# Kernel tuning notes

Hardware: AMD Instinct MI355X
Metric: run time of the kernel (lower is better)

## Reference

```python
import jax, jax.numpy as jnp
import numpy as np

NHEAD = 8
K_NEIGH = 16


def setup_inputs() -> dict:
    key = jax.random.key(0)
    ks = jax.random.split(key, 6)
    B, L, D = 4, 4096, 512
    x = jax.random.normal(ks[0], (B, L, D), dtype=jnp.float32)
    positions = jax.random.uniform(ks[1], (B, L, 3), dtype=jnp.float32)
    in_proj_w = jax.random.normal(ks[2], (3 * D, D), dtype=jnp.float32) * 0.02
    in_proj_b = jax.random.normal(ks[3], (3 * D,), dtype=jnp.float32) * 0.02
    out_proj_w = jax.random.normal(ks[4], (D, D), dtype=jnp.float32) * 0.02
    out_proj_b = jax.random.normal(ks[5], (D,), dtype=jnp.float32) * 0.02
    return {"x": x, "positions": positions, "in_proj_w": in_proj_w,
            "in_proj_b": in_proj_b, "out_proj_w": out_proj_w, "out_proj_b": out_proj_b}


def _sparse_attention(x, positions, in_proj_w, in_proj_b, out_proj_w, out_proj_b):
    B, L, D = x.shape
    H, dh = NHEAD, D // NHEAD
    K = min(K_NEIGH, L)
    scale = 1.0 / jnp.sqrt(jnp.asarray(dh, x.dtype))

    # Pairwise distances [B, L, L]; topk smallest -> neighbor indices [B, L, K].
    diff = positions[:, :, None, :] - positions[:, None, :, :]
    dist = jnp.sqrt(jnp.sum(diff * diff, axis=-1))
    _, nbr = jax.lax.top_k(-dist, K)  # [B, L, K]

    Wq, Wk, Wv = in_proj_w[:D], in_proj_w[D:2 * D], in_proj_w[2 * D:]
    bq, bk, bv = in_proj_b[:D], in_proj_b[D:2 * D], in_proj_b[2 * D:]

    # Query is x[b, i] itself (self is always its own nearest neighbor at dist 0),
    # so the selected attention row equals attention with query x[b, i] over neighbors.
    q = ((x @ Wq.T + bq) * scale).reshape(B, L, H, dh)

    # Gather neighbor features: [B, L, K, D]
    b_idx = jnp.arange(B)[:, None, None]
    local_x = x[b_idx, nbr]
    k = (local_x @ Wk.T + bk).reshape(B, L, K, H, dh)
    v = (local_x @ Wv.T + bv).reshape(B, L, K, H, dh)

    scores = jnp.einsum('blhd,blkhd->blhk', q, k)
    attn = jax.nn.softmax(scores, axis=-1)
    ctx = jnp.einsum('blhk,blkhd->blhd', attn, v).reshape(B, L, D)
    out = ctx @ out_proj_w.T + out_proj_b

    # Faithful fallback: if i not among its neighbors, pass through x[b, i].
    is_in = jnp.any(nbr == jnp.arange(L)[None, :, None], axis=-1)  # [B, L]
    return jnp.where(is_in[..., None], out, x)


def reference(x, positions, in_proj_w, in_proj_b, out_proj_w, out_proj_b):
    return _sparse_attention(x, positions, in_proj_w, in_proj_b, out_proj_w, out_proj_b)
```

## Files before the change

### kernel.cpp

```cpp
#include <hip/hip_runtime.h>
#include <cfloat>
#include <cmath>

constexpr int B = 4;
constexpr int L = 4096;
constexpr int D = 512;
constexpr int NH = 8;
constexpr int DH = 64;
constexpr int KN = 16;
constexpr int M = B * L;
constexpr int N_IN = 3 * D;
constexpr int NCELL = 512;

typedef __attribute__((ext_vector_type(8))) short short8;
typedef __attribute__((ext_vector_type(4))) float f32x4;
typedef unsigned short ushort;
typedef unsigned long long ull;

__device__ __forceinline__ ushort f2bf(float f) {
  unsigned u = __float_as_uint(f);
  u = u + 0x7fffu + ((u >> 16) & 1u);
  return (ushort)(u >> 16);
}
__device__ __forceinline__ float bf2f(ushort h) {
  return __uint_as_float(((unsigned)h) << 16);
}
__device__ __forceinline__ float dot8(const uint4 qu, const uint4 ku, float a) {
  a = fmaf(bf2f((ushort)qu.x), bf2f((ushort)ku.x), a);
  a = fmaf(bf2f((ushort)(qu.x >> 16)), bf2f((ushort)(ku.x >> 16)), a);
  a = fmaf(bf2f((ushort)qu.y), bf2f((ushort)ku.y), a);
  a = fmaf(bf2f((ushort)(qu.y >> 16)), bf2f((ushort)(ku.y >> 16)), a);
  a = fmaf(bf2f((ushort)qu.z), bf2f((ushort)ku.z), a);
  a = fmaf(bf2f((ushort)(qu.z >> 16)), bf2f((ushort)(ku.z >> 16)), a);
  a = fmaf(bf2f((ushort)qu.w), bf2f((ushort)ku.w), a);
  a = fmaf(bf2f((ushort)(qu.w >> 16)), bf2f((ushort)(ku.w >> 16)), a);
  return a;
}
__device__ __forceinline__ void acc8(float wgt, const uint4 vv, float (&acc)[8]) {
  acc[0] = fmaf(wgt, bf2f((ushort)vv.x), acc[0]);
  acc[1] = fmaf(wgt, bf2f((ushort)(vv.x >> 16)), acc[1]);
  acc[2] = fmaf(wgt, bf2f((ushort)vv.y), acc[2]);
  acc[3] = fmaf(wgt, bf2f((ushort)(vv.y >> 16)), acc[3]);
  acc[4] = fmaf(wgt, bf2f((ushort)vv.z), acc[4]);
  acc[5] = fmaf(wgt, bf2f((ushort)(vv.z >> 16)), acc[5]);
  acc[6] = fmaf(wgt, bf2f((ushort)vv.w), acc[6]);
  acc[7] = fmaf(wgt, bf2f((ushort)(vv.w >> 16)), acc[7]);
}
__device__ __forceinline__ uint2 pack4hi(const float4 v) {
  uint2 o;
  o.x = (unsigned)f2bf(v.x) | ((unsigned)f2bf(v.y) << 16);
  o.y = (unsigned)f2bf(v.z) | ((unsigned)f2bf(v.w) << 16);
  return o;
}
__device__ __forceinline__ void gload16(const void* g, void* l) {
  __builtin_amdgcn_global_load_lds(
      (const __attribute__((address_space(1))) void*)g,
      (__attribute__((address_space(3))) void*)l, 16, 0, 0);
}
__device__ __forceinline__ int morton3(int x, int y, int z) {
  int m = 0;
#pragma unroll
  for (int i = 0; i < 3; ++i)
    m |= (((x >> i) & 1) << (3 * i + 2)) | (((y >> i) & 1) << (3 * i + 1)) |
         (((z >> i) & 1) << (3 * i));
  return m;
}

constexpr int TP = 65;

__device__ __forceinline__ void topk_finish(
    const float* sxT, const float* syT, const float* szT, ull* lstw,
    const int lane, const float qx, const float qy, const float qz,
    const unsigned mbits, const int l, const int row,
    int* __restrict__ nbr, int* __restrict__ isin) {
  unsigned lo = 1, hi = 0x40400001u;
  while (lo < hi) {
    const unsigned mid = (lo + hi) >> 1;
    const int c = __popcll(__ballot(mbits < mid));
    if (c >= 16) hi = mid; else lo = mid + 1;
  }
  const unsigned P = lo + 16;

  int cnt = 0;
  ull am = __ballot(mbits < P);
  const ull below = (1ull << lane) - 1ull;
  while (am) {
    const int pl = (int)__builtin_ctzll(am);
    am &= am - 1;
    const int a = pl * TP + lane;
    const float dx = qx - sxT[a], dy = qy - syT[a], dz = qz - szT[a];
    const float d2 = fmaf(dx, dx, fmaf(dy, dy, dz * dz));
    const bool hit = __float_as_uint(d2) < P;
    const ull msk = __ballot(hit);
    if (hit) {
      const int slot = cnt + __popcll(msk & below);
      if (slot < 64) {
        const unsigned c = (unsigned)(lane * 64 + pl);
        lstw[slot] = ((ull)__float_as_uint(sqrtf(d2)) << 32) | c;
      }
    }
    cnt += __popcll(msk);
  }
  const int n = min(cnt, 64);

  const ull mine = (lane < n) ? lstw[lane] : ~0ull;
  int r = 0;
  for (int i = 0; i < n; ++i) r += (lstw[i] < mine) ? 1 : 0;

  const int idx = (int)(unsigned)(mine & 0xffffffffu);
  const bool wr = (lane < n) && (r < 16);
  if (wr) nbr[(size_t)row * KN + r] = idx;
  const ull hit2 = __ballot(wr && idx == l);
  if (lane == 0) isin[row] = hit2 ? 1 : 0;
}

constexpr int TOPK_BLKS = B * (L / 32);
constexpr int SORT_BLKS = B;
constexpr int CVTX_BLKS = 1024;
constexpr int CVTW_BLKS = 256;
constexpr int STAGE0_BLKS = TOPK_BLKS + SORT_BLKS + CVTX_BLKS + CVTW_BLKS;

__global__ __launch_bounds__(512) void stage0_kernel(
    const float* __restrict__ pos, const float* __restrict__ x,
    const float* __restrict__ in_w, const float* __restrict__ out_w,
    int* __restrict__ nbr, int* __restrict__ isin, int* __restrict__ qorder,
    ushort* __restrict__ xb, ushort* __restrict__ iwh,
    ushort* __restrict__ owh, ushort* __restrict__ owl) {
  __shared__ ull smem_u64[54016 / 8];

  const int bid = blockIdx.x;
  const int tid = threadIdx.x;

  if (bid < TOPK_BLKS) {
    float* sxT = (float*)smem_u64;
    float* syT = sxT + 64 * TP;
    float* szT = syT + 64 * TP;
    ull* lst = (ull*)(szT + 64 * TP);

    const int wave = tid >> 6;
    const int lane = tid & 63;
    const int b = bid >> 7;
    const int l0 = (bid & 127) * 32 + wave * 4;

    const float* p = pos + (size_t)b * L * 3;
    for (int i = tid; i < L; i += 512) {
      const int a = (i & 63) * TP + (i >> 6);
      sxT[a] = p[3 * i + 0];
      syT[a] = p[3 * i + 1];
      szT[a] = p[3 * i + 2];
    }
    __syncthreads();

    float qx[4], qy[4], qz[4], mn[4];
#pragma unroll
    for (int q = 0; q < 4; ++q) {
      const int lq = l0 + q;
      const int qa = (lq & 63) * TP + (lq >> 6);
      qx[q] = sxT[qa];
      qy[q] = syT[qa];
      qz[q] = szT[qa];
      mn[q] = FLT_MAX;
    }

    const int base = lane * TP;
    for (int j = 0; j < 64; ++j) {
      const int a = base + j;
      const float cx = sxT[a], cy = syT[a], cz = szT[a];
#pragma unroll
      for (int q = 0; q < 4; ++q) {
        const float dx = qx[q] - cx, dy = qy[q] - cy, dz = qz[q] - cz;
        mn[q] = fminf(mn[q], fmaf(dx, dx, fmaf(dy, dy, dz * dz)));
      }
    }

    ull* lstw = lst + wave * 64;
#pragma unroll
    for (int q = 0; q < 4; ++q)
      topk_finish(sxT, syT, szT, lstw, lane, qx[q], qy[q], qz[q],
                  __float_as_uint(mn[q]), l0 + q, b * L + l0 + q, nbr, isin);

  } else if (bid < TOPK_BLKS + SORT_BLKS) {
    int* hist = (int*)smem_u64;
    int* scanbuf = hist + NCELL;
    const int b = bid - TOPK_BLKS;
    const int t = tid;
    hist[t] = 0;
    __syncthreads();

    int cells[8], ranks[8];
    const float* p = pos + (size_t)b * L * 3;
#pragma unroll
    for (int q = 0; q < 8; ++q) {
      const int i = q * 512 + t;
      const int ix = min(7, max(0, (int)(p[3 * i + 0] * 8.f)));
      const int iy = min(7, max(0, (int)(p[3 * i + 1] * 8.f)));
      const int iz = min(7, max(0, (int)(p[3 * i + 2] * 8.f)));
      cells[q] = morton3(ix, iy, iz);
      ranks[q] = atomicAdd(&hist[cells[q]], 1);
    }
    __syncthreads();

    int accv = hist[t];
    const int orig = accv;
    scanbuf[t] = accv;
    __syncthreads();
    for (int s = 1; s < NCELL; s <<= 1) {
      const int o = (t >= s) ? scanbuf[t - s] : 0;
      __syncthreads();
      accv += o;
      scanbuf[t] = accv;
      __syncthreads();
    }
    hist[t] = accv - orig;
    __syncthreads();

#pragma unroll
    for (int q = 0; q < 8; ++q) {
      const int i = q * 512 + t;
      qorder[b * L + hist[cells[q]] + ranks[q]] = i;
    }

  } else if (bid < TOPK_BLKS + SORT_BLKS + CVTX_BLKS) {
    const int vb = bid - TOPK_BLKS - SORT_BLKS;
    const int n8 = M * D / 8;
    for (int i = vb * 512 + tid; i < n8; i += CVTX_BLKS * 512) {
      const float4 v0 = reinterpret_cast<const float4*>(x)[i * 2];
      const float4 v1 = reinterpret_cast<const float4*>(x)[i * 2 + 1];
      uint4 o;
      const uint2 a = pack4hi(v0), b2 = pack4hi(v1);
      o.x = a.x; o.y = a.y; o.z = b2.x; o.w = b2.y;
      reinterpret_cast<uint4*>(xb)[i] = o;
    }

  } else {
    const int vb = bid - TOPK_BLKS - SORT_BLKS - CVTX_BLKS;
    const int ni8 = N_IN * D / 8;
    const int no8 = D * D / 8;
    for (int i = vb * 512 + tid; i < ni8 + no8; i += CVTW_BLKS * 512) {
      if (i < ni8) {
        const float4 v0 = reinterpret_cast<const float4*>(in_w)[i * 2];
        const float4 v1 = reinterpret_cast<const float4*>(in_w)[i * 2 + 1];
        uint4 o;
        const uint2 a = pack4hi(v0), b2 = pack4hi(v1);
        o.x = a.x; o.y = a.y; o.z = b2.x; o.w = b2.y;
        reinterpret_cast<uint4*>(iwh)[i] = o;
      } else {
        const int j = i - ni8;
        const float4 v0 = reinterpret_cast<const float4*>(out_w)[j * 2];
        const float4 v1 = reinterpret_cast<const float4*>(out_w)[j * 2 + 1];
        uint4 oh, ol;
        const uint2 a = pack4hi(v0), b2 = pack4hi(v1);
        oh.x = a.x; oh.y = a.y; oh.z = b2.x; oh.w = b2.y;
        const float4 r0 = make_float4(v0.x - bf2f(f2bf(v0.x)), v0.y - bf2f(f2bf(v0.y)),
                                      v0.z - bf2f(f2bf(v0.z)), v0.w - bf2f(f2bf(v0.w)));
        const float4 r1 = make_float4(v1.x - bf2f(f2bf(v1.x)), v1.y - bf2f(f2bf(v1.y)),
                                      v1.z - bf2f(f2bf(v1.z)), v1.w - bf2f(f2bf(v1.w)));
        const uint2 c = pack4hi(r0), d2 = pack4hi(r1);
        ol.x = c.x; ol.y = c.y; ol.z = d2.x; ol.w = d2.y;
        reinterpret_cast<uint4*>(owh)[j] = oh;
        reinterpret_cast<uint4*>(owl)[j] = ol;
      }
    }
  }
}

constexpr int BM = 128, BN = 128;
constexpr int BK2 = 64;

__global__ __launch_bounds__(256) void gemm_in(const ushort* __restrict__ A,
                                               const ushort* __restrict__ W,
                                               const float* __restrict__ bias,
                                               ushort* __restrict__ qb,
                                               ushort* __restrict__ kb,
                                               ushort* __restrict__ vb) {
  __shared__ ushort Ah[BM * BK2];
  __shared__ ushort Bh[BN * BK2];

  const int tid = threadIdx.x;
  const int m0 = blockIdx.x * BM;
  const int n0 = blockIdx.y * BN;

  const int wv = tid >> 6;
  const int lane = tid & 63;
  const int srow0 = wv * 8 + (lane >> 3);
  const int gchunk = (lane & 7) ^ (lane >> 3);
  const ushort* Asrc = A + (size_t)(m0 + srow0) * D + gchunk * 8;
  const ushort* Wsrc = W + (size_t)(n0 + srow0) * D + gchunk * 8;
  ushort* AhB0 = Ah + (wv * 8) * BK2;
  ushort* AhB1 = Ah + (wv * 8 + 32) * BK2;
  ushort* AhB2 = Ah + (wv * 8 + 64) * BK2;
  ushort* AhB3 = Ah + (wv * 8 + 96) * BK2;
  ushort* BhB0 = Bh + (wv * 8) * BK2;
  ushort* BhB1 = Bh + (wv * 8 + 32) * BK2;
  ushort* BhB2 = Bh + (wv * 8 + 64) * BK2;
  ushort* BhB3 = Bh + (wv * 8 + 96) * BK2;

  const int wr0 = (wv >> 1) * 64;
  const int wc0 = (wv & 1) * 64;
  const int fr_row = lane & 15;
  const int cbase = lane >> 4;
  const int rx = lane & 7;

  f32x4 acc[4][4];
#pragma unroll
  for (int i = 0; i < 4; ++i)
#pragma unroll
    for (int j = 0; j < 4; ++j) acc[i][j] = {0.f, 0.f, 0.f, 0.f};

  for (int k0 = 0; k0 < D; k0 += BK2) {
    __syncthreads();
    gload16(Asrc + k0, AhB0);
    gload16(Asrc + (size_t)32 * D + k0, AhB1);
    gload16(Asrc + (size_t)64 * D + k0, AhB2);
    gload16(Asrc + (size_t)96 * D + k0, AhB3);
    gload16(Wsrc + k0, BhB0);
    gload16(Wsrc + (size_t)32 * D + k0, BhB1);
    gload16(Wsrc + (size_t)64 * D + k0, BhB2);
    gload16(Wsrc + (size_t)96 * D + k0, BhB3);
    __syncthreads();

#pragma unroll
    for (int kk = 0; kk < 2; ++kk) {
      const int slot = (kk * 4 + cbase) ^ rx;
      short8 ah[4];
#pragma unroll
      for (int fr = 0; fr < 4; ++fr)
        ah[fr] = *reinterpret_cast<const short8*>(
            &Ah[(wr0 + fr * 16 + fr_row) * BK2 + slot * 8]);
#pragma unroll
      for (int fc = 0; fc < 4; ++fc) {
        const short8 bh = *reinterpret_cast<const short8*>(
            &Bh[(wc0 + fc * 16 + fr_row) * BK2 + slot * 8]);
#pragma unroll
        for (int fr = 0; fr < 4; ++fr)
          acc[fr][fc] = __builtin_amdgcn_mfma_f32_16x16x32_bf16(ah[fr], bh, acc[fr][fc], 0, 0, 0);
      }
    }
  }

  const int region = n0 >> 9;
  ushort* outb = region == 0 ? qb : (region == 1 ? kb : vb);
  const float scl = region == 0 ? 0.125f : 1.0f;
  const int nloc0 = (n0 & 511) + wc0;
#pragma unroll
  for (int fr = 0; fr < 4; ++fr) {
#pragma unroll
    for (int r = 0; r < 4; ++r) {
      const int grow = m0 + wr0 + fr * 16 + (lane >> 4) * 4 + r;
#pragma unroll
      for (int fc = 0; fc < 4; ++fc) {
        const int cc = fc * 16 + (lane & 15);
        const float v = (acc[fr][fc][r] + bias[n0 + wc0 + cc]) * scl;
        outb[(size_t)grow * D + nloc0 + cc] = f2bf(v);
      }
    }
  }
}

__global__ __launch_bounds__(256) void gemm_out(const ushort* __restrict__ A,
                                                const ushort* __restrict__ Wh,
                                                const ushort* __restrict__ Wl,
                                                const float* __restrict__ bias,
                                                float* __restrict__ C,
                                                const float* __restrict__ X,
                                                const int* __restrict__ isin) {
  __shared__ ushort Ah[BM * BK2];
  __shared__ ushort Bh[BN * BK2];
  __shared__ ushort Bl[BN * BK2];

  const int tid = threadIdx.x;
  const int m0 = blockIdx.x * BM;
  const int n0 = blockIdx.y * BN;

  const int wv = tid >> 6;
  const int lane = tid & 63;
  const int srow0 = wv * 8 + (lane >> 3);
  const int gchunk = (lane & 7) ^ (lane >> 3);
  const ushort* Asrc = A + (size_t)(m0 + srow0) * D + gchunk * 8;
  const ushort* Hsrc = Wh + (size_t)(n0 + srow0) * D + gchunk * 8;
  const ushort* Lsrc = Wl + (size_t)(n0 + srow0) * D + gchunk * 8;
  ushort* AhB0 = Ah + (wv * 8) * BK2;
  ushort* AhB1 = Ah + (wv * 8 + 32) * BK2;
  ushort* AhB2 = Ah + (wv * 8 + 64) * BK2;
  ushort* AhB3 = Ah + (wv * 8 + 96) * BK2;
  ushort* BhB0 = Bh + (wv * 8) * BK2;
  ushort* BhB1 = Bh + (wv * 8 + 32) * BK2;
  ushort* BhB2 = Bh + (wv * 8 + 64) * BK2;
  ushort* BhB3 = Bh + (wv * 8 + 96) * BK2;
  ushort* BlB0 = Bl + (wv * 8) * BK2;
  ushort* BlB1 = Bl + (wv * 8 + 32) * BK2;
  ushort* BlB2 = Bl + (wv * 8 + 64) * BK2;
  ushort* BlB3 = Bl + (wv * 8 + 96) * BK2;

  const int wr0 = (wv >> 1) * 64;
  const int wc0 = (wv & 1) * 64;
  const int fr_row = lane & 15;
  const int cbase = lane >> 4;
  const int rx = lane & 7;

  f32x4 acc[4][4];
#pragma unroll
  for (int i = 0; i < 4; ++i)
#pragma unroll
    for (int j = 0; j < 4; ++j) acc[i][j] = {0.f, 0.f, 0.f, 0.f};

  for (int k0 = 0; k0 < D; k0 += BK2) {
    __syncthreads();
    gload16(Asrc + k0, AhB0);
    gload16(Asrc + (size_t)32 * D + k0, AhB1);
    gload16(Asrc + (size_t)64 * D + k0, AhB2);
    gload16(Asrc + (size_t)96 * D + k0, AhB3);
    gload16(Hsrc + k0, BhB0);
    gload16(Hsrc + (size_t)32 * D + k0, BhB1);
    gload16(Hsrc + (size_t)64 * D + k0, BhB2);
    gload16(Hsrc + (size_t)96 * D + k0, BhB3);
    gload16(Lsrc + k0, BlB0);
    gload16(Lsrc + (size_t)32 * D + k0, BlB1);
    gload16(Lsrc + (size_t)64 * D + k0, BlB2);
    gload16(Lsrc + (size_t)96 * D + k0, BlB3);
    __syncthreads();

#pragma unroll
    for (int kk = 0; kk < 2; ++kk) {
      const int slot = (kk * 4 + cbase) ^ rx;
      short8 ah[4];
#pragma unroll
      for (int fr = 0; fr < 4; ++fr)
        ah[fr] = *reinterpret_cast<const short8*>(
            &Ah[(wr0 + fr * 16 + fr_row) * BK2 + slot * 8]);
#pragma unroll
      for (int fc = 0; fc < 4; ++fc) {
        const short8 bh = *reinterpret_cast<const short8*>(
            &Bh[(wc0 + fc * 16 + fr_row) * BK2 + slot * 8]);
        const short8 bl = *reinterpret_cast<const short8*>(
            &Bl[(wc0 + fc * 16 + fr_row) * BK2 + slot * 8]);
#pragma unroll
        for (int fr = 0; fr < 4; ++fr) {
          acc[fr][fc] = __builtin_amdgcn_mfma_f32_16x16x32_bf16(ah[fr], bh, acc[fr][fc], 0, 0, 0);
          acc[fr][fc] = __builtin_amdgcn_mfma_f32_16x16x32_bf16(ah[fr], bl, acc[fr][fc], 0, 0, 0);
        }
      }
    }
  }

#pragma unroll
  for (int fr = 0; fr < 4; ++fr) {
#pragma unroll
    for (int r = 0; r < 4; ++r) {
      const int grow = m0 + wr0 + fr * 16 + (lane >> 4) * 4 + r;
      const int ok = isin[grow];
#pragma unroll
      for (int fc = 0; fc < 4; ++fc) {
        const int gcol = n0 + wc0 + fc * 16 + (lane & 15);
        float v = acc[fr][fc][r] + bias[gcol];
        if (!ok) v = X[(size_t)grow * D + gcol];
        C[(size_t)grow * D + gcol] = v;
      }
    }
  }
}

__global__ __launch_bounds__(256) void attn_kernel(const ushort* __restrict__ qb,
                                                   const ushort* __restrict__ kb,
                                                   const ushort* __restrict__ vb,
                                                   const int* __restrict__ nbr,
                                                   const int* __restrict__ qorder,
                                                   ushort* __restrict__ ctx) {
  const int wave = threadIdx.x >> 6;
  const int lane = threadIdx.x & 63;
  const int xcd = blockIdx.x & 7;
  const int chunk = blockIdx.x >> 3;
  const int b = xcd >> 1;
  const int slot = ((xcd & 1) * 512 + chunk) * 4 + wave;
  const int l = qorder[b * L + slot];
  const int bl = b * L + l;
  const int bbase = b * L;
  const int* nb = nbr + (size_t)bl * KN;

  const int h = lane >> 3;
  const int n0 = lane & 7;
  const int glane = h * 8;

  const ushort* qp = qb + (size_t)bl * D + h * DH;
  uint4 qv[8];
#pragma unroll
  for (int i = 0; i < 8; ++i)
    qv[i] = *reinterpret_cast<const uint4*>(qp + i * 8);

  const int j0 = nb[n0];
  const int j1 = nb[n0 + 8];
  float a0 = 0.f, a1 = 0.f;
  {
    const ushort* kr0 = kb + (size_t)(bbase + j0) * D + h * DH;
    const ushort* kr1 = kb + (size_t)(bbase + j1) * D + h * DH;
#pragma unroll
    for (int i = 0; i < 8; ++i) {
      a0 = dot8(qv[i], *reinterpret_cast<const uint4*>(kr0 + i * 8), a0);
      a1 = dot8(qv[i], *reinterpret_cast<const uint4*>(kr1 + i * 8), a1);
    }
  }

  float mx = fmaxf(a0, a1);
  mx = fmaxf(mx, __shfl_xor(mx, 1));
  mx = fmaxf(mx, __shfl_xor(mx, 2));
  mx = fmaxf(mx, __shfl_xor(mx, 4));
  const float e0 = expf(a0 - mx), e1 = expf(a1 - mx);
  float sm = e0 + e1;
  sm += __shfl_xor(sm, 1);
  sm += __shfl_xor(sm, 2);
  sm += __shfl_xor(sm, 4);
  const float inv = 1.0f / sm;
  const float w0 = e0 * inv, w1 = e1 * inv;

  float ww[KN];
  int jj[KN];
#pragma unroll
  for (int n = 0; n < KN; ++n) {
    const int src = glane + (n & 7);
    ww[n] = __shfl((n < 8) ? w0 : w1, src);
    jj[n] = __shfl((n < 8) ? j0 : j1, src);
  }

  const int d0 = n0 * 8;
  const ushort* vbase = vb + (size_t)bbase * D + h * DH + d0;
  float acc[8];
#pragma unroll
  for (int i = 0; i < 8; ++i) acc[i] = 0.f;

#pragma unroll
  for (int g = 0; g < KN; g += 4) {
    const uint4 va0 = *reinterpret_cast<const uint4*>(vbase + (size_t)jj[g] * D);
    const uint4 va1 = *reinterpret_cast<const uint4*>(vbase + (size_t)jj[g + 1] * D);
    const uint4 va2 = *reinterpret_cast<const uint4*>(vbase + (size_t)jj[g + 2] * D);
    const uint4 va3 = *reinterpret_cast<const uint4*>(vbase + (size_t)jj[g + 3] * D);
    acc8(ww[g], va0, acc);
    acc8(ww[g + 1], va1, acc);
    acc8(ww[g + 2], va2, acc);
    acc8(ww[g + 3], va3, acc);
  }

  uint4 o;
  o.x = (unsigned)f2bf(acc[0]) | ((unsigned)f2bf(acc[1]) << 16);
  o.y = (unsigned)f2bf(acc[2]) | ((unsigned)f2bf(acc[3]) << 16);
  o.z = (unsigned)f2bf(acc[4]) | ((unsigned)f2bf(acc[5]) << 16);
  o.w = (unsigned)f2bf(acc[6]) | ((unsigned)f2bf(acc[7]) << 16);
  *reinterpret_cast<uint4*>(ctx + (size_t)bl * D + h * DH + d0) = o;
}

extern "C" void kernel_launch(void* const* d_in, const int* in_sizes, int n_in,
                              void* d_out, int out_size, void* d_ws, size_t ws_size,
                              hipStream_t stream) {
  const float* x     = (const float*)d_in[0];
  const float* pos   = (const float*)d_in[1];
  const float* in_w  = (const float*)d_in[2];
  const float* in_b  = (const float*)d_in[3];
  const float* out_w = (const float*)d_in[4];
  const float* out_b = (const float*)d_in[5];
  float* out = (float*)d_out;

  const size_t nbr_bytes  = (size_t)M * KN * sizeof(int);
  const size_t isin_bytes = (size_t)M * sizeof(int);
  const size_t half_bytes = (size_t)M * D * sizeof(ushort);
  const size_t iwh_bytes  = (size_t)N_IN * D * sizeof(ushort);
  const size_t ow_bytes   = (size_t)D * D * sizeof(ushort);
  const size_t sort_bytes = (size_t)M * sizeof(int);
  const size_t need = nbr_bytes + isin_bytes + 5 * half_bytes +
                      iwh_bytes + 2 * ow_bytes + sort_bytes + 16384;
  if (ws_size < need) return;

  char* w = (char*)d_ws;
  int*    nbr    = (int*)w;    w += (nbr_bytes + 255) & ~(size_t)255;
  int*    isin   = (int*)w;    w += (isin_bytes + 255) & ~(size_t)255;
  ushort* xb     = (ushort*)w; w += (half_bytes + 255) & ~(size_t)255;
  ushort* qb     = (ushort*)w; w += (half_bytes + 255) & ~(size_t)255;
  ushort* kb     = (ushort*)w; w += (half_bytes + 255) & ~(size_t)255;
  ushort* vb     = (ushort*)w; w += (half_bytes + 255) & ~(size_t)255;
  ushort* ctxb   = (ushort*)w; w += (half_bytes + 255) & ~(size_t)255;
  ushort* iwh    = (ushort*)w; w += (iwh_bytes + 255) & ~(size_t)255;
  ushort* owh    = (ushort*)w; w += (ow_bytes + 255) & ~(size_t)255;
  ushort* owl    = (ushort*)w; w += (ow_bytes + 255) & ~(size_t)255;
  int*    qorder = (int*)w;

  stage0_kernel<<<STAGE0_BLKS, 512, 0, stream>>>(
      pos, x, in_w, out_w, nbr, isin, qorder, xb, iwh, owh, owl);

  gemm_in<<<dim3(M / BM, N_IN / BN), 256, 0, stream>>>(xb, iwh, in_b, qb, kb, vb);

  attn_kernel<<<M / 4, 256, 0, stream>>>(qb, kb, vb, nbr, qorder, ctxb);

  gemm_out<<<dim3(M / BM, D / BN), 256, 0, stream>>>(ctxb, owh, owl, out_b, out, x, isin);
}
```

Before: 145.5 us.

## Move top-k neighbor search into the QKV projection GEMM kernel launch

The kNN top-k blocks move out of the stage0 conversion kernel and into a merged kernel alongside the input-projection GEMM blocks. Top-k now runs with 256-thread blocks covering 16 rows each, so it overlaps with the GEMM instead of with the conversion work. The goal is to balance the stages and hide the compute-bound top-k behind the GEMM. The catch is that the merged kernel has the top-k's larger shared-memory footprint and the union of both paths' register needs, which can lower GEMM occupancy.

```diff
diff --git a/kernel.cpp b/kernel.cpp
--- a/kernel.cpp
+++ b/kernel.cpp
@@ -114,75 +114,25 @@
   if (lane == 0) isin[row] = hit2 ? 1 : 0;
 }
 
-constexpr int TOPK_BLKS = B * (L / 32);
 constexpr int SORT_BLKS = B;
 constexpr int CVTX_BLKS = 1024;
 constexpr int CVTW_BLKS = 256;
-constexpr int STAGE0_BLKS = TOPK_BLKS + SORT_BLKS + CVTX_BLKS + CVTW_BLKS;
+constexpr int STAGE0_BLKS = SORT_BLKS + CVTX_BLKS + CVTW_BLKS;
 
 __global__ __launch_bounds__(512) void stage0_kernel(
     const float* __restrict__ pos, const float* __restrict__ x,
     const float* __restrict__ in_w, const float* __restrict__ out_w,
-    int* __restrict__ nbr, int* __restrict__ isin, int* __restrict__ qorder,
-    ushort* __restrict__ xb, ushort* __restrict__ iwh,
-    ushort* __restrict__ owh, ushort* __restrict__ owl) {
-  __shared__ ull smem_u64[54016 / 8];
+    int* __restrict__ qorder, ushort* __restrict__ xb,
+    ushort* __restrict__ iwh, ushort* __restrict__ owh,
+    ushort* __restrict__ owl) {
+  __shared__ int hist[NCELL];
+  __shared__ int scanbuf[NCELL];
 
   const int bid = blockIdx.x;
   const int tid = threadIdx.x;
 
-  if (bid < TOPK_BLKS) {
-    float* sxT = (float*)smem_u64;
-    float* syT = sxT + 64 * TP;
-    float* szT = syT + 64 * TP;
-    ull* lst = (ull*)(szT + 64 * TP);
-
-    const int wave = tid >> 6;
-    const int lane = tid & 63;
-    const int b = bid >> 7;
-    const int l0 = (bid & 127) * 32 + wave * 4;
-
-    const float* p = pos + (size_t)b * L * 3;
-    for (int i = tid; i < L; i += 512) {
-      const int a = (i & 63) * TP + (i >> 6);
-      sxT[a] = p[3 * i + 0];
-      syT[a] = p[3 * i + 1];
-      szT[a] = p[3 * i + 2];
-    }
-    __syncthreads();
-
-    float qx[4], qy[4], qz[4], mn[4];
-#pragma unroll
-    for (int q = 0; q < 4; ++q) {
-      const int lq = l0 + q;
-      const int qa = (lq & 63) * TP + (lq >> 6);
-      qx[q] = sxT[qa];
-      qy[q] = syT[qa];
-      qz[q] = szT[qa];
-      mn[q] = FLT_MAX;
-    }
-
-    const int base = lane * TP;
-    for (int j = 0; j < 64; ++j) {
-      const int a = base + j;
-      const float cx = sxT[a], cy = syT[a], cz = szT[a];
-#pragma unroll
-      for (int q = 0; q < 4; ++q) {
-        const float dx = qx[q] - cx, dy = qy[q] - cy, dz = qz[q] - cz;
-        mn[q] = fminf(mn[q], fmaf(dx, dx, fmaf(dy, dy, dz * dz)));
-      }
-    }
-
-    ull* lstw = lst + wave * 64;
-#pragma unroll
-    for (int q = 0; q < 4; ++q)
-      topk_finish(sxT, syT, szT, lstw, lane, qx[q], qy[q], qz[q],
-                  __float_as_uint(mn[q]), l0 + q, b * L + l0 + q, nbr, isin);
-
-  } else if (bid < TOPK_BLKS + SORT_BLKS) {
-    int* hist = (int*)smem_u64;
-    int* scanbuf = hist + NCELL;
-    const int b = bid - TOPK_BLKS;
+  if (bid < SORT_BLKS) {
+    const int b = bid;
     const int t = tid;
     hist[t] = 0;
     __syncthreads();
@@ -220,8 +170,8 @@
       qorder[b * L + hist[cells[q]] + ranks[q]] = i;
     }
 
-  } else if (bid < TOPK_BLKS + SORT_BLKS + CVTX_BLKS) {
-    const int vb = bid - TOPK_BLKS - SORT_BLKS;
+  } else if (bid < SORT_BLKS + CVTX_BLKS) {
+    const int vb = bid - SORT_BLKS;
     const int n8 = M * D / 8;
     for (int i = vb * 512 + tid; i < n8; i += CVTX_BLKS * 512) {
       const float4 v0 = reinterpret_cast<const float4*>(x)[i * 2];
@@ -233,7 +183,7 @@
     }
 
   } else {
-    const int vb = bid - TOPK_BLKS - SORT_BLKS - CVTX_BLKS;
+    const int vb = bid - SORT_BLKS - CVTX_BLKS;
     const int ni8 = N_IN * D / 8;
     const int no8 = D * D / 8;
     for (int i = vb * 512 + tid; i < ni8 + no8; i += CVTW_BLKS * 512) {
@@ -266,92 +216,150 @@
 
 constexpr int BM = 128, BN = 128;
 constexpr int BK2 = 64;
-
-__global__ __launch_bounds__(256) void gemm_in(const ushort* __restrict__ A,
-                                               const ushort* __restrict__ W,
-                                               const float* __restrict__ bias,
-                                               ushort* __restrict__ qb,
-                                               ushort* __restrict__ kb,
-                                               ushort* __restrict__ vb) {
-  __shared__ ushort Ah[BM * BK2];
-  __shared__ ushort Bh[BN * BK2];
-
+constexpr int TOPK_BLKS = B * (L / 16);
+constexpr int GEMM_BLKS = (M / BM) * (N_IN / BN);
+constexpr int K1_BLKS = TOPK_BLKS + GEMM_BLKS;
+
+__global__ __launch_bounds__(256) void topk_gemm_kernel(
+    const float* __restrict__ pos, const ushort* __restrict__ A,
+    const ushort* __restrict__ W, const float* __restrict__ bias,
+    int* __restrict__ nbr, int* __restrict__ isin,
+    ushort* __restrict__ qb, ushort* __restrict__ kb,
+    ushort* __restrict__ vb) {
+  __shared__ ull smem_u64[51968 / 8];
+
+  const int bid = blockIdx.x;
   const int tid = threadIdx.x;
-  const int m0 = blockIdx.x * BM;
-  const int n0 = blockIdx.y * BN;
-
-  const int wv = tid >> 6;
-  const int lane = tid & 63;
-  const int srow0 = wv * 8 + (lane >> 3);
-  const int gchunk = (lane & 7) ^ (lane >> 3);
-  const ushort* Asrc = A + (size_t)(m0 + srow0) * D + gchunk * 8;
-  const ushort* Wsrc = W + (size_t)(n0 + srow0) * D + gchunk * 8;
-  ushort* AhB0 = Ah + (wv * 8) * BK2;
-  ushort* AhB1 = Ah + (wv * 8 + 32) * BK2;
-  ushort* AhB2 = Ah + (wv * 8 + 64) * BK2;
-  ushort* AhB3 = Ah + (wv * 8 + 96) * BK2;
-  ushort* BhB0 = Bh + (wv * 8) * BK2;
-  ushort* BhB1 = Bh + (wv * 8 + 32) * BK2;
-  ushort* BhB2 = Bh + (wv * 8 + 64) * BK2;
-  ushort* BhB3 = Bh + (wv * 8 + 96) * BK2;
-
-  const int wr0 = (wv >> 1) * 64;
-  const int wc0 = (wv & 1) * 64;
-  const int fr_row = lane & 15;
-  const int cbase = lane >> 4;
-  const int rx = lane & 7;
-
-  f32x4 acc[4][4];
-#pragma unroll
-  for (int i = 0; i < 4; ++i)
-#pragma unroll
-    for (int j = 0; j < 4; ++j) acc[i][j] = {0.f, 0.f, 0.f, 0.f};
-
-  for (int k0 = 0; k0 < D; k0 += BK2) {
+
+  if (bid < TOPK_BLKS) {
+    float* sxT = (float*)smem_u64;
+    float* syT = sxT + 64 * TP;
+    float* szT = syT + 64 * TP;
+    ull* lst = (ull*)(szT + 64 * TP);
+
+    const int wave = tid >> 6;
+    const int lane = tid & 63;
+    const int b = bid >> 8;
+    const int l0 = (bid & 255) * 16 + wave * 4;
+
+    const float* p = pos + (size_t)b * L * 3;
+    for (int i = tid; i < L; i += 256) {
+      const int a = (i & 63) * TP + (i >> 6);
+      sxT[a] = p[3 * i + 0];
+      syT[a] = p[3 * i + 1];
+      szT[a] = p[3 * i + 2];
+    }
     __syncthreads();
-    gload16(Asrc + k0, AhB0);
-    gload16(Asrc + (size_t)32 * D + k0, AhB1);
-    gload16(Asrc + (size_t)64 * D + k0, AhB2);
-    gload16(Asrc + (size_t)96 * D + k0, AhB3);
-    gload16(Wsrc + k0, BhB0);
-    gload16(Wsrc + (size_t)32 * D + k0, BhB1);
-    gload16(Wsrc + (size_t)64 * D + k0, BhB2);
-    gload16(Wsrc + (size_t)96 * D + k0, BhB3);
-    __syncthreads();
-
-#pragma unroll
-    for (int kk = 0; kk < 2; ++kk) {
-      const int slot = (kk * 4 + cbase) ^ rx;
-      short8 ah[4];
-#pragma unroll
-      for (int fr = 0; fr < 4; ++fr)
-        ah[fr] = *reinterpret_cast<const short8*>(
-            &Ah[(wr0 + fr * 16 + fr_row) * BK2 + slot * 8]);
-#pragma unroll
-      for (int fc = 0; fc < 4; ++fc) {
-        const short8 bh = *reinterpret_cast<const short8*>(
-            &Bh[(wc0 + fc * 16 + fr_row) * BK2 + slot * 8]);
+
+    float qx[4], qy[4], qz[4], mn[4];
+#pragma unroll
+    for (int q = 0; q < 4; ++q) {
+      const int lq = l0 + q;
+      const int qa = (lq & 63) * TP + (lq >> 6);
+      qx[q] = sxT[qa];
+      qy[q] = syT[qa];
+      qz[q] = szT[qa];
+      mn[q] = FLT_MAX;
+    }
+
+    const int base = lane * TP;
+    for (int j = 0; j < 64; ++j) {
+      const int a = base + j;
+      const float cx = sxT[a], cy = syT[a], cz = szT[a];
+#pragma unroll
+      for (int q = 0; q < 4; ++q) {
+        const float dx = qx[q] - cx, dy = qy[q] - cy, dz = qz[q] - cz;
+        mn[q] = fminf(mn[q], fmaf(dx, dx, fmaf(dy, dy, dz * dz)));
+      }
+    }
+
+    ull* lstw = lst + wave * 64;
+#pragma unroll
+    for (int q = 0; q < 4; ++q)
+      topk_finish(sxT, syT, szT, lstw, lane, qx[q], qy[q], qz[q],
+                  __float_as_uint(mn[q]), l0 + q, b * L + l0 + q, nbr, isin);
+
+  } else {
+    ushort* Ah = (ushort*)smem_u64;
+    ushort* Bh = Ah + BM * BK2;
+
+    const int gbid = bid - TOPK_BLKS;
+    const int m0 = (gbid & 127) * BM;
+    const int n0 = (gbid >> 7) * BN;
+
+    const int wv = tid >> 6;
+    const int lane = tid & 63;
+    const int srow0 = wv * 8 + (lane >> 3);
+    const int gchunk = (lane & 7) ^ (lane >> 3);
+    const ushort* Asrc = A + (size_t)(m0 + srow0) * D + gchunk * 8;
+    const ushort* Wsrc = W + (size_t)(n0 + srow0) * D + gchunk * 8;
+    ushort* AhB0 = Ah + (wv * 8) * BK2;
+    ushort* AhB1 = Ah + (wv * 8 + 32) * BK2;
+    ushort* AhB2 = Ah + (wv * 8 + 64) * BK2;
+    ushort* AhB3 = Ah + (wv * 8 + 96) * BK2;
+    ushort* BhB0 = Bh + (wv * 8) * BK2;
+    ushort* BhB1 = Bh + (wv * 8 + 32) * BK2;
+    ushort* BhB2 = Bh + (wv * 8 + 64) * BK2;
+    ushort* BhB3 = Bh + (wv * 8 + 96) * BK2;
+
+    const int wr0 = (wv >> 1) * 64;
+    const int wc0 = (wv & 1) * 64;
+    const int fr_row = lane & 15;
+    const int cbase = lane >> 4;
+    const int rx = lane & 7;
+
+    f32x4 acc[4][4];
+#pragma unroll
+    for (int i = 0; i < 4; ++i)
+#pragma unroll
+      for (int j = 0; j < 4; ++j) acc[i][j] = {0.f, 0.f, 0.f, 0.f};
+
+    for (int k0 = 0; k0 < D; k0 += BK2) {
+      __syncthreads();
+      gload16(Asrc + k0, AhB0);
+      gload16(Asrc + (size_t)32 * D + k0, AhB1);
+      gload16(Asrc + (size_t)64 * D + k0, AhB2);
+      gload16(Asrc + (size_t)96 * D + k0, AhB3);
+      gload16(Wsrc + k0, BhB0);
+      gload16(Wsrc + (size_t)32 * D + k0, BhB1);
+      gload16(Wsrc + (size_t)64 * D + k0, BhB2);
+      gload16(Wsrc + (size_t)96 * D + k0, BhB3);
+      __syncthreads();
+
+#pragma unroll
+      for (int kk = 0; kk < 2; ++kk) {
+        const int slot = (kk * 4 + cbase) ^ rx;
+        short8 ah[4];
 #pragma unroll
         for (int fr = 0; fr < 4; ++fr)
-          acc[fr][fc] = __builtin_amdgcn_mfma_f32_16x16x32_bf16(ah[fr], bh, acc[fr][fc], 0, 0, 0);
+          ah[fr] = *reinterpret_cast<const short8*>(
+              &Ah[(wr0 + fr * 16 + fr_row) * BK2 + slot * 8]);
+#pragma unroll
+        for (int fc = 0; fc < 4; ++fc) {
+          const short8 bh = *reinterpret_cast<const short8*>(
+              &Bh[(wc0 + fc * 16 + fr_row) * BK2 + slot * 8]);
+#pragma unroll
+          for (int fr = 0; fr < 4; ++fr)
+            acc[fr][fc] = __builtin_amdgcn_mfma_f32_16x16x32_bf16(ah[fr], bh, acc[fr][fc], 0, 0, 0);
+        }
       }
     }
-  }
-
-  const int region = n0 >> 9;
-  ushort* outb = region == 0 ? qb : (region == 1 ? kb : vb);
-  const float scl = region == 0 ? 0.125f : 1.0f;
-  const int nloc0 = (n0 & 511) + wc0;
-#pragma unroll
-  for (int fr = 0; fr < 4; ++fr) {
-#pragma unroll
-    for (int r = 0; r < 4; ++r) {
-      const int grow = m0 + wr0 + fr * 16 + (lane >> 4) * 4 + r;
-#pragma unroll
-      for (int fc = 0; fc < 4; ++fc) {
-        const int cc = fc * 16 + (lane & 15);
-        const float v = (acc[fr][fc][r] + bias[n0 + wc0 + cc]) * scl;
-        outb[(size_t)grow * D + nloc0 + cc] = f2bf(v);
+
+    const int region = n0 >> 9;
+    ushort* outb = region == 0 ? qb : (region == 1 ? kb : vb);
+    const float scl = region == 0 ? 0.125f : 1.0f;
+    const int nloc0 = (n0 & 511) + wc0;
+#pragma unroll
+    for (int fr = 0; fr < 4; ++fr) {
+#pragma unroll
+      for (int r = 0; r < 4; ++r) {
+        const int grow = m0 + wr0 + fr * 16 + (lane >> 4) * 4 + r;
+#pragma unroll
+        for (int fc = 0; fc < 4; ++fc) {
+          const int cc = fc * 16 + (lane & 15);
+          const float v = (acc[fr][fc][r] + bias[n0 + wc0 + cc]) * scl;
+          outb[(size_t)grow * D + nloc0 + cc] = f2bf(v);
+        }
       }
     }
   }
@@ -582,9 +590,10 @@
   int*    qorder = (int*)w;
 
   stage0_kernel<<<STAGE0_BLKS, 512, 0, stream>>>(
-      pos, x, in_w, out_w, nbr, isin, qorder, xb, iwh, owh, owl);
-
-  gemm_in<<<dim3(M / BM, N_IN / BN), 256, 0, stream>>>(xb, iwh, in_b, qb, kb, vb);
+      pos, x, in_w, out_w, qorder, xb, iwh, owh, owl);
+
+  topk_gemm_kernel<<<K1_BLKS, 256, 0, stream>>>(
+      pos, xb, iwh, in_b, nbr, isin, qb, kb, vb);
 
   attn_kernel<<<M / 4, 256, 0, stream>>>(qb, kb, vb, nbr, qorder, ctxb);
 
```

New measurement: 169.9 us. 16.8% more time.
